# Performance work log

Measured on AMD Instinct MI355X. Metric: run time of the kernel, lower is better.

Reference implementation:

```python
import jax, jax.numpy as jnp
import numpy as np

B, C, H, W = 8, 256, 64, 64
NH, FF, L, K = 8, 1024, 3, 64
THR = 0.5
DH = C // NH
SCALE = 1.0 / float(np.sqrt(DH))
N = H * W


def setup_inputs() -> dict:
    key = jax.random.key(0)
    ks = jax.random.split(key, 16)
    s = 0.02
    rn = lambda k, shape: (jax.random.normal(k, shape, jnp.float32) * s)
    return {
        "x": jax.random.normal(ks[0], (B, C, H, W), jnp.float32),
        "y": jax.random.normal(ks[1], (B, C, H, W), jnp.float32),
        "proj_w": rn(ks[2], (C, 2 * C)), "proj_b": rn(ks[3], (C,)),
        "sal_w": rn(ks[4], (1, C)), "sal_b": rn(ks[5], (1,)),
        "soft_w": rn(ks[6], (2, K, C)), "soft_b": rn(ks[7], (2, K)),
        "attn_in_w": rn(ks[8], (2, L, 3 * C, C)), "attn_in_b": rn(ks[9], (2, L, 3 * C)),
        "attn_out_w": rn(ks[10], (2, L, C, C)), "attn_out_b": rn(ks[11], (2, L, C)),
        "n1_g": jnp.ones((2, L, C), jnp.float32), "n1_b": jnp.zeros((2, L, C), jnp.float32),
        "ffn_w1": rn(ks[12], (2, L, FF, C)), "ffn_b1": rn(ks[13], (2, L, FF)),
        "ffn_w2": rn(ks[14], (2, L, C, FF)), "ffn_b2": rn(ks[15], (2, L, C)),
        "n2_g": jnp.ones((2, L, C), jnp.float32), "n2_b": jnp.zeros((2, L, C), jnp.float32),
    }


def _ln(t, g, b, eps=1e-5):
    m = t.mean(-1, keepdims=True)
    v = ((t - m) ** 2).mean(-1, keepdims=True)
    return (t - m) / jnp.sqrt(v + eps) * g + b


def _layers(q, kv, p, side):
    # q: [B,N,C] pixel queries, kv: [B,K,C] soft-pooled tokens
    for l in range(L):
        iw, ib = p["attn_in_w"][side, l], p["attn_in_b"][side, l]
        qq = (q @ iw[:C].T + ib[:C]).reshape(B, -1, NH, DH)
        kk = (kv @ iw[C:2 * C].T + ib[C:2 * C]).reshape(B, K, NH, DH)
        vv = (kv @ iw[2 * C:].T + ib[2 * C:]).reshape(B, K, NH, DH)
        att = jax.nn.softmax(jnp.einsum('bnhd,bkhd->bhnk', qq, kk) * SCALE, axis=-1)
        o = jnp.einsum('bhnk,bkhd->bnhd', att, vv).reshape(B, -1, C)
        o = o @ p["attn_out_w"][side, l].T + p["attn_out_b"][side, l]
        q = _ln(q + o, p["n1_g"][side, l], p["n1_b"][side, l])
        h = jax.nn.relu(q @ p["ffn_w1"][side, l].T + p["ffn_b1"][side, l])
        h = h @ p["ffn_w2"][side, l].T + p["ffn_b2"][side, l]
        q = _ln(q + h, p["n2_g"][side, l], p["n2_b"][side, l])
    return q


def _forward(x, y, proj_w, proj_b, sal_w, sal_b, soft_w, soft_b,
             attn_in_w, attn_in_b, attn_out_w, attn_out_b, n1_g, n1_b,
             ffn_w1, ffn_b1, ffn_w2, ffn_b2, n2_g, n2_b):
    p = dict(attn_in_w=attn_in_w, attn_in_b=attn_in_b, attn_out_w=attn_out_w,
             attn_out_b=attn_out_b, n1_g=n1_g, n1_b=n1_b, ffn_w1=ffn_w1,
             ffn_b1=ffn_b1, ffn_w2=ffn_w2, ffn_b2=ffn_b2, n2_g=n2_g, n2_b=n2_b)
    xc = jnp.concatenate([x, y], axis=1)                                  # [B,2C,H,W]
    feat = jnp.einsum('oc,bchw->bohw', proj_w, xc) + proj_b[None, :, None, None]
    sal = jnp.einsum('oc,bchw->bohw', sal_w, feat) + sal_b[None, :, None, None]  # [B,1,H,W]
    heat = jax.nn.sigmoid(sal)
    fg_mask = (heat >= THR).reshape(B, 1, N)
    bg_mask = (heat < 1.0 - THR).reshape(B, 1, N)
    fmap = feat.reshape(B, C, N)
    q0 = fmap.transpose(0, 2, 1)                                          # [B,N,C]
    out = fmap
    for side, hm in ((0, heat), (1, 1.0 - heat)):
        wf = feat * hm                                                    # [B,C,H,W]
        sw = (jnp.einsum('kc,bchw->bkhw', soft_w[side], wf)
              + soft_b[side][None, :, None, None]).reshape(B, K, N)       # [B,K,N]
        pool = jnp.einsum('bkn,bcn->bkc', sw, wf.reshape(B, C, N))        # [B,K,C]
        qs = _layers(q0, pool, p, side)                                   # [B,N,C]
        mask = fg_mask if side == 0 else bg_mask
        out = jnp.where(mask, qs.transpose(0, 2, 1), out)
    # per-image skip: if no fg or no bg pixels, keep original feature
    valid = fg_mask.any(axis=(1, 2)) & bg_mask.any(axis=(1, 2))           # [B]
    out = jnp.where(valid[:, None, None], out, fmap)
    return out.reshape(B, C, H, W)


def reference(x, y, proj_w, proj_b, sal_w, sal_b, soft_w, soft_b,
              attn_in_w, attn_in_b, attn_out_w, attn_out_b, n1_g, n1_b,
              ffn_w1, ffn_b1, ffn_w2, ffn_b2, n2_g, n2_b):
    return _forward(x, y, proj_w, proj_b, sal_w, sal_b, soft_w, soft_b,
                    attn_in_w, attn_in_b, attn_out_w, attn_out_b, n1_g, n1_b,
                    ffn_w1, ffn_b1, ffn_w2, ffn_b2, n2_g, n2_b)
```

## Files before the change

### kernel.cpp

```cpp
#include <hip/hip_runtime.h>
#include <stdint.h>

#define B_ 8
#define C_ 256
#define N_ 4096
#define K_ 64
#define NH_ 8
#define FF_ 1024
#define L_ 3
#define M_ (B_*N_)
#define SCALE_ 0.17677669529663687f

typedef float f32x4 __attribute__((ext_vector_type(4)));
typedef __bf16 v8bf __attribute__((ext_vector_type(8)));

__device__ __forceinline__ float b2f(unsigned short h){
  union { uint32_t u; float f; } v; v.u = ((uint32_t)h) << 16; return v.f;
}
__device__ __forceinline__ unsigned short f2b(float f){
  union { float f; uint32_t u; } v; v.f = f;
  uint32_t r = v.u + 0x7fffu + ((v.u >> 16) & 1u);
  return (unsigned short)(r >> 16);
}
__device__ __forceinline__ void gload_lds16(const void* g, void* l){
  __builtin_amdgcn_global_load_lds(
      (const __attribute__((address_space(1))) unsigned int*)g,
      (__attribute__((address_space(3))) unsigned int*)l, 16, 0, 0);
}

__global__ __launch_bounds__(256) void k_f32_to_bf16(const float* __restrict__ src,
                                                     unsigned short* __restrict__ dst, int n){
  int i4 = (blockIdx.x*256 + threadIdx.x)*4;
  if (i4 >= n) return;
  float4 v = *(const float4*)(src + i4);
  uint32_t p0 = (uint32_t)f2b(v.x) | ((uint32_t)f2b(v.y) << 16);
  uint32_t p1 = (uint32_t)f2b(v.z) | ((uint32_t)f2b(v.w) << 16);
  *(uint2*)(dst + i4) = make_uint2(p0, p1);
}

__global__ __launch_bounds__(256) void k_build_xcT(const float* __restrict__ x,
                                                   const float* __restrict__ y,
                                                   unsigned short* __restrict__ xcT){
  __shared__ float t[32][33];
  int b = blockIdx.z;
  int n0 = blockIdx.x*32, c0 = blockIdx.y*32;
  int tx = threadIdx.x, ty = threadIdx.y;
  const float* src = (c0 < 256) ? (x + ((size_t)b*256 + c0)*N_)
                                : (y + ((size_t)b*256 + (c0-256))*N_);
  #pragma unroll
  for (int i = 0; i < 4; i++){
    int cl = ty*4 + i;
    t[cl][tx] = src[(size_t)cl*N_ + n0 + tx];
  }
  __syncthreads();
  #pragma unroll
  for (int i = 0; i < 4; i++){
    int nl = ty*4 + i;
    xcT[((size_t)b*N_ + n0 + nl)*512 + c0 + tx] = f2b(t[tx][nl]);
  }
}

__global__ __launch_bounds__(256) void k_featmir(const float* __restrict__ featT,
                                                 unsigned short* __restrict__ featbf,
                                                 unsigned short* __restrict__ featC){
  __shared__ float t[32][33];
  int b = blockIdx.z;
  int n0 = blockIdx.x*32, c0 = blockIdx.y*32;
  int tx = threadIdx.x, ty = threadIdx.y;
  #pragma unroll
  for (int i = 0; i < 4; i++){
    int nl = ty*4 + i;
    size_t m = (size_t)b*N_ + n0 + nl;
    float v = featT[m*256 + c0 + tx];
    t[nl][tx] = v;
    featbf[m*256 + c0 + tx] = f2b(v);
  }
  __syncthreads();
  #pragma unroll
  for (int i = 0; i < 4; i++){
    int cl = ty*4 + i;
    featC[((size_t)b*256 + c0 + cl)*(size_t)N_ + n0 + tx] = f2b(t[tx][cl]);
  }
}

__global__ __launch_bounds__(512) void k_compute_u(const float* __restrict__ sal_w,
                                                   const float* __restrict__ proj_w,
                                                   const float* __restrict__ proj_b,
                                                   const float* __restrict__ sal_b,
                                                   double* __restrict__ u){
  int c2 = threadIdx.x;
  double acc = 0.0;
  for (int c = 0; c < 256; ++c)
    acc += (double)sal_w[c] * (double)proj_w[(size_t)c*512 + c2];
  u[c2] = acc;
  if (c2 == 0){
    double s0 = (double)sal_b[0];
    for (int c = 0; c < 256; ++c) s0 += (double)sal_w[c] * (double)proj_b[c];
    u[512] = s0;
  }
}

__global__ __launch_bounds__(256) void k_sal_heat(const float* __restrict__ x,
                                                  const float* __restrict__ y,
                                                  const double* __restrict__ u,
                                                  float* __restrict__ heat,
                                                  int* __restrict__ counts){
  int pix = blockIdx.x*256 + threadIdx.x;
  int b = pix >> 12, n = pix & 4095;
  const float* xb = x + (size_t)b*256*N_ + n;
  const float* yb = y + (size_t)b*256*N_ + n;
  double acc = u[512];
  for (int c = 0; c < 256; ++c) acc += u[c]     * (double)xb[(size_t)c*N_];
  for (int c = 0; c < 256; ++c) acc += u[256+c] * (double)yb[(size_t)c*N_];
  float hf = (float)(1.0 / (1.0 + exp(-acc)));
  heat[pix] = hf;
  unsigned long long mfg = __ballot(hf >= 0.5f);
  unsigned long long mbg = __ballot(hf < 0.5f);
  if ((threadIdx.x & 63) == 0){
    atomicAdd(&counts[b*2+0], (int)__popcll(mfg));
    atomicAdd(&counts[b*2+1], (int)__popcll(mbg));
  }
}

template<int EPI>
__global__ __launch_bounds__(256) void k_gemm_bt(
    const unsigned short* __restrict__ A, const unsigned short* __restrict__ W,
    const float* __restrict__ bias, void* __restrict__ out,
    int M, int N, int K){
  __shared__ unsigned short smem[2][2][128*64];
  int tid = threadIdx.x;
  int w = tid >> 6, l = tid & 63;
  int m0 = blockIdx.x * 128, n0 = blockIdx.y * 128;
  int wr = w >> 1, wc = w & 1;
  int lr = l & 15, lk = l >> 4;
  f32x4 acc[4][4] = {};
  int nt = K >> 6;
  #pragma unroll
  for (int i = 0; i < 4; i++){
    int idx = i*256 + tid;
    int row = idx >> 3, su = ((idx & 7) ^ (row & 7))*8;
    gload_lds16(A + (size_t)(m0+row)*K + su, &smem[0][0][idx*8]);
    gload_lds16(W + (size_t)(n0+row)*K + su, &smem[0][1][idx*8]);
  }
  __syncthreads();
  for (int t = 0; t < nt; ++t){
    int cur = t & 1;
    if (t + 1 < nt){
      int k0 = (t + 1) << 6;
      #pragma unroll
      for (int i = 0; i < 4; i++){
        int idx = i*256 + tid;
        int row = idx >> 3, su = ((idx & 7) ^ (row & 7))*8;
        gload_lds16(A + (size_t)(m0+row)*K + k0 + su, &smem[cur^1][0][idx*8]);
        gload_lds16(W + (size_t)(n0+row)*K + k0 + su, &smem[cur^1][1][idx*8]);
      }
    }
    const unsigned short* ldsA = smem[cur][0];
    const unsigned short* ldsB = smem[cur][1];
    #pragma unroll
    for (int kk = 0; kk < 2; kk++){
      v8bf af[4], bfr[4];
      #pragma unroll
      for (int f = 0; f < 4; f++){
        int ra = wr*64 + f*16 + lr;
        int rb2 = wc*64 + f*16 + lr;
        int u = kk*4 + lk;
        af[f]  = *(const v8bf*)(&ldsA[ra*64 + ((u ^ (ra&7))<<3)]);
        bfr[f] = *(const v8bf*)(&ldsB[rb2*64 + ((u ^ (rb2&7))<<3)]);
      }
      #pragma unroll
      for (int fi = 0; fi < 4; fi++)
        #pragma unroll
        for (int fj = 0; fj < 4; fj++)
          acc[fi][fj] = __builtin_amdgcn_mfma_f32_16x16x32_bf16(af[fi], bfr[fj], acc[fi][fj], 0, 0, 0);
    }
    __syncthreads();
  }
  if (EPI == 1 || EPI == 2){
    unsigned short* st = &smem[0][0][0];
    #pragma unroll
    for (int fj = 0; fj < 4; fj++){
      int col = wc*64 + fj*16 + lr;
      float bv = bias[n0 + col];
      #pragma unroll
      for (int fi = 0; fi < 4; fi++){
        int rl = wr*64 + fi*16 + lk*4;
        #pragma unroll
        for (int r = 0; r < 4; r++){
          float v = acc[fi][fj][r] + bv;
          if (EPI == 1) v = fmaxf(v, 0.f);
          st[(rl + r)*136 + col] = f2b(v);
        }
      }
    }
    __syncthreads();
    #pragma unroll
    for (int it = 0; it < 8; it++){
      int idx = it*256 + tid;
      int row = idx >> 4, c8 = (idx & 15)*8;
      *(uint4*)((unsigned short*)out + (size_t)(m0+row)*N + n0 + c8)
          = *(const uint4*)&st[row*136 + c8];
    }
  } else {
    #pragma unroll
    for (int fj = 0; fj < 4; fj++){
      int col = n0 + wc*64 + fj*16 + lr;
      float bv = bias[col];
      #pragma unroll
      for (int fi = 0; fi < 4; fi++){
        int rb = m0 + wr*64 + fi*16 + lk*4;
        #pragma unroll
        for (int r = 0; r < 4; r++){
          float v = acc[fi][fj][r] + bv;
          if (EPI == 3){
            int row = rb + r;
            ((unsigned short*)out)[((size_t)(row>>6)*256 + col)*64 + (row&63)] = f2b(v);
          } else {
            ((float*)out)[(size_t)(rb + r)*N + col] = v;
          }
        }
      }
    }
  }
}

__global__ __launch_bounds__(256) void k_swh(const float* __restrict__ g_all,
                                             const float* __restrict__ heat,
                                             const float* __restrict__ soft_b,
                                             unsigned short* __restrict__ swh){
  __shared__ float gl[64*129];
  __shared__ float hml[64];
  int tid = threadIdx.x;
  int blk = blockIdx.x;
  size_t m0 = (size_t)blk*64;
  int b = (int)(m0 >> 12), n0 = (int)(m0 & 4095);
  #pragma unroll
  for (int i = 0; i < 32; i++){
    int idx = i*256 + tid;
    int row = idx >> 7, col = idx & 127;
    gl[row*129 + col] = g_all[(m0 + row)*128 + col];
  }
  if (tid < 64) hml[tid] = heat[(size_t)b*4096 + n0 + tid];
  __syncthreads();
  int k = tid >> 2, j0 = (tid & 3)*16;
  #pragma unroll
  for (int s = 0; s < 2; s++){
    float sb = soft_b[s*64 + k];
    unsigned short vals[16];
    #pragma unroll
    for (int j = 0; j < 16; j++){
      int n = j0 + j;
      float h = hml[n];
      float hm = s ? (1.0f - h) : h;
      vals[j] = f2b((gl[n*129 + s*64 + k]*hm + sb)*hm);
    }
    unsigned short* dst = swh + (((size_t)b*2 + s)*64 + k)*4096 + n0 + j0;
    uint4 o0, o1;
    o0.x = vals[0] | ((uint32_t)vals[1]<<16);  o0.y = vals[2] | ((uint32_t)vals[3]<<16);
    o0.z = vals[4] | ((uint32_t)vals[5]<<16);  o0.w = vals[6] | ((uint32_t)vals[7]<<16);
    o1.x = vals[8] | ((uint32_t)vals[9]<<16);  o1.y = vals[10]| ((uint32_t)vals[11]<<16);
    o1.z = vals[12]| ((uint32_t)vals[13]<<16); o1.w = vals[14]| ((uint32_t)vals[15]<<16);
    *(uint4*)dst = o0;
    *(uint4*)(dst + 8) = o1;
  }
}

__global__ __launch_bounds__(256) void k_poolgemm(
    const unsigned short* __restrict__ swh, const unsigned short* __restrict__ featC,
    float* __restrict__ pp){
  __shared__ unsigned short ldsA[128*64];
  __shared__ unsigned short ldsB[128*64];
  int tid = threadIdx.x;
  int w = tid >> 6, l = tid & 63;
  int kc = blockIdx.x, nt = blockIdx.y, b = blockIdx.z;
  int wr = w >> 1, wc = w & 1;
  int lr = l & 15, lk = l >> 4;
  const unsigned short* A = swh  + (size_t)b*128*4096 + kc*512;
  const unsigned short* W = featC + ((size_t)b*256 + nt*128)*4096 + kc*512;
  f32x4 acc[4][4] = {};
  for (int k0 = 0; k0 < 512; k0 += 64){
    #pragma unroll
    for (int i = 0; i < 4; i++){
      int idx = i*256 + tid;
      int row = idx >> 3, su = (idx & 7) ^ (row & 7);
      gload_lds16(A + (size_t)row*4096 + k0 + su*8, &ldsA[idx*8]);
    }
    #pragma unroll
    for (int i = 0; i < 4; i++){
      int idx = i*256 + tid;
      int row = idx >> 3, su = (idx & 7) ^ (row & 7);
      gload_lds16(W + (size_t)row*4096 + k0 + su*8, &ldsB[idx*8]);
    }
    __syncthreads();
    #pragma unroll
    for (int kk = 0; kk < 2; kk++){
      v8bf af[4], bfr[4];
      #pragma unroll
      for (int f = 0; f < 4; f++){
        int ra = wr*64 + f*16 + lr;
        int rb2 = wc*64 + f*16 + lr;
        int u = kk*4 + lk;
        af[f]  = *(const v8bf*)(&ldsA[ra*64 + ((u ^ (ra&7))<<3)]);
        bfr[f] = *(const v8bf*)(&ldsB[rb2*64 + ((u ^ (rb2&7))<<3)]);
      }
      #pragma unroll
      for (int fi = 0; fi < 4; fi++)
        #pragma unroll
        for (int fj = 0; fj < 4; fj++)
          acc[fi][fj] = __builtin_amdgcn_mfma_f32_16x16x32_bf16(af[fi], bfr[fj], acc[fi][fj], 0, 0, 0);
    }
    __syncthreads();
  }
  float* dst = pp + ((size_t)kc*8 + b)*128*256;
  #pragma unroll
  for (int fj = 0; fj < 4; fj++){
    int col = nt*128 + wc*64 + fj*16 + lr;
    #pragma unroll
    for (int fi = 0; fi < 4; fi++){
      int rb = wr*64 + fi*16 + lk*4;
      #pragma unroll
      for (int r = 0; r < 4; r++)
        dst[(size_t)(rb + r)*256 + col] = acc[fi][fj][r];
    }
  }
}

__global__ __launch_bounds__(256) void k_pool2b(const float* __restrict__ pp,
                                                unsigned short* __restrict__ pool_bf_s){
  int bk = blockIdx.x, side = blockIdx.y, c = threadIdx.x;
  int b = bk >> 6, k = bk & 63;
  float s = 0.f;
  #pragma unroll
  for (int kc = 0; kc < 8; kc++)
    s += pp[(((size_t)kc*8 + b)*128 + side*64 + k)*256 + c];
  pool_bf_s[((size_t)side*512 + bk)*256 + c] = f2b(s);
}

__global__ __launch_bounds__(256) void k_attn2(
    const unsigned short* __restrict__ qq, const unsigned short* __restrict__ kk,
    const unsigned short* __restrict__ vvT, unsigned short* __restrict__ obf){
  __shared__ unsigned short sk[64*256];
  __shared__ unsigned short svT[256*64];
  __shared__ unsigned short sp[4][16*64];
  __shared__ unsigned short sow[4][16*32];
  int tid = threadIdx.x, w = tid >> 6, l = tid & 63;
  int blk = blockIdx.x, b = blk >> 6;
  int l15 = l & 15, lg = l >> 4;
  const uint4* ksrc = (const uint4*)(kk + (size_t)b*64*256);
  #pragma unroll
  for (int i = 0; i < 8; i++){
    int u = i*256 + tid;
    int row = u >> 5, j = u & 31;
    *(uint4*)&sk[row*256 + ((j ^ (row&7))<<3)] = ksrc[u];
  }
  const uint4* vsrc = (const uint4*)(vvT + (size_t)b*256*64);
  #pragma unroll
  for (int i = 0; i < 8; i++){
    int u = i*256 + tid;
    int row = u >> 3, j = u & 7;
    *(uint4*)&svT[row*64 + ((j ^ (row&7))<<3)] = vsrc[u];
  }
  __syncthreads();
  size_t qrow = (size_t)blk*64 + w*16 + l15;
  for (int h = 0; h < 8; h++){
    v8bf aq = *(const v8bf*)(qq + qrow*256 + h*32 + lg*8);
    f32x4 s[4];
    #pragma unroll
    for (int kt = 0; kt < 4; kt++){
      int row = kt*16 + l15;
      v8bf bk = *(const v8bf*)&sk[row*256 + (((h*4 + lg) ^ (row&7))<<3)];
      f32x4 z = {};
      s[kt] = __builtin_amdgcn_mfma_f32_16x16x32_bf16(aq, bk, z, 0, 0, 0);
    }
    #pragma unroll
    for (int r = 0; r < 4; r++){
      float v0 = s[0][r]*SCALE_, v1 = s[1][r]*SCALE_;
      float v2 = s[2][r]*SCALE_, v3 = s[3][r]*SCALE_;
      float mx = fmaxf(fmaxf(v0, v1), fmaxf(v2, v3));
      mx = fmaxf(mx, __shfl_xor(mx, 1));
      mx = fmaxf(mx, __shfl_xor(mx, 2));
      mx = fmaxf(mx, __shfl_xor(mx, 4));
      mx = fmaxf(mx, __shfl_xor(mx, 8));
      float e0 = __expf(v0-mx), e1 = __expf(v1-mx);
      float e2 = __expf(v2-mx), e3 = __expf(v3-mx);
      float sum = e0+e1+e2+e3;
      sum += __shfl_xor(sum, 1); sum += __shfl_xor(sum, 2);
      sum += __shfl_xor(sum, 4); sum += __shfl_xor(sum, 8);
      float inv = 1.0f/sum;
      s[0][r] = e0*inv; s[1][r] = e1*inv; s[2][r] = e2*inv; s[3][r] = e3*inv;
    }
    #pragma unroll
    for (int kt = 0; kt < 4; kt++){
      int colu = kt*2 + (l15>>3);
      #pragma unroll
      for (int r = 0; r < 4; r++){
        int row = lg*4 + r;
        sp[w][row*64 + ((colu ^ (row&7))<<3) + (l&7)] = f2b(s[kt][r]);
      }
    }
    f32x4 o[2] = {};
    #pragma unroll
    for (int k2 = 0; k2 < 2; k2++){
      v8bf pa = *(const v8bf*)&sp[w][l15*64 + (((k2*4 + lg) ^ (l15&7))<<3)];
      #pragma unroll
      for (int dt = 0; dt < 2; dt++){
        int vrow = h*32 + dt*16 + l15;
        v8bf bv = *(const v8bf*)&svT[vrow*64 + (((k2*4 + lg) ^ (vrow&7))<<3)];
        o[dt] = __builtin_amdgcn_mfma_f32_16x16x32_bf16(pa, bv, o[dt], 0, 0, 0);
      }
    }
    #pragma unroll
    for (int dt = 0; dt < 2; dt++)
      #pragma unroll
      for (int r = 0; r < 4; r++)
        sow[w][(lg*4 + r)*32 + dt*16 + l15] = f2b(o[dt][r]);
    uint4 ov = *(const uint4*)&sow[w][l15*32 + lg*8];
    *(uint4*)(obf + qrow*256 + h*32 + lg*8) = ov;
  }
}

template<int RF32>
__global__ __launch_bounds__(256) void k_ln2(
    const void* __restrict__ resid, const unsigned short* __restrict__ delta,
    const float* __restrict__ g, const float* __restrict__ bta,
    unsigned short* __restrict__ qout){
  int wv = threadIdx.x >> 6, l = threadIdx.x & 63;
  size_t m = (size_t)blockIdx.x*4 + wv;
  uint2 dv = *(const uint2*)(delta + m*256 + l*4);
  float d0 = b2f((unsigned short)(dv.x & 0xffff)), d1 = b2f((unsigned short)(dv.x >> 16));
  float d2 = b2f((unsigned short)(dv.y & 0xffff)), d3 = b2f((unsigned short)(dv.y >> 16));
  float x0, x1, x2, x3;
  if (RF32){
    float4 rv = *(const float4*)((const float*)resid + m*256 + l*4);
    x0 = rv.x+d0; x1 = rv.y+d1; x2 = rv.z+d2; x3 = rv.w+d3;
  } else {
    uint2 rv = *(const uint2*)((const unsigned short*)resid + m*256 + l*4);
    x0 = b2f((unsigned short)(rv.x & 0xffff)) + d0;
    x1 = b2f((unsigned short)(rv.x >> 16)) + d1;
    x2 = b2f((unsigned short)(rv.y & 0xffff)) + d2;
    x3 = b2f((unsigned short)(rv.y >> 16)) + d3;
  }
  float s = x0+x1+x2+x3;
  float ss = x0*x0+x1*x1+x2*x2+x3*x3;
  #pragma unroll
  for (int off = 32; off; off >>= 1){
    s  += __shfl_xor(s, off);
    ss += __shfl_xor(ss, off);
  }
  float mean = s * (1.0f/256.0f);
  float var = ss * (1.0f/256.0f) - mean*mean;
  float rstd = 1.0f / sqrtf(var + 1e-5f);
  float4 gv = *(const float4*)(g + l*4);
  float4 bv = *(const float4*)(bta + l*4);
  float y0 = (x0-mean)*rstd*gv.x + bv.x;
  float y1 = (x1-mean)*rstd*gv.y + bv.y;
  float y2 = (x2-mean)*rstd*gv.z + bv.z;
  float y3 = (x3-mean)*rstd*gv.w + bv.w;
  uint32_t p0 = (uint32_t)f2b(y0) | ((uint32_t)f2b(y1)<<16);
  uint32_t p1 = (uint32_t)f2b(y2) | ((uint32_t)f2b(y3)<<16);
  *(uint2*)(qout + m*256 + l*4) = make_uint2(p0,p1);
}

__global__ __launch_bounds__(256) void k_select(
    const unsigned short* __restrict__ qA, const unsigned short* __restrict__ qB,
    const float* __restrict__ featT, const float* __restrict__ heat,
    const int* __restrict__ counts, float* __restrict__ out){
  __shared__ float t[32][33];
  int b = blockIdx.z;
  int n0 = blockIdx.x*32, c0 = blockIdx.y*32;
  int tx = threadIdx.x, ty = threadIdx.y;
  bool valid = (counts[b*2] > 0) && (counts[b*2+1] > 0);
  #pragma unroll
  for (int i = 0; i < 4; i++){
    int nl = ty*4+i;
    size_t m = (size_t)b*4096 + n0 + nl;
    float v;
    if (!valid) v = featT[m*256 + c0 + tx];
    else {
      bool fg = heat[(size_t)b*4096 + n0 + nl] >= 0.5f;
      v = fg ? b2f(qA[m*256 + c0 + tx]) : b2f(qB[m*256 + c0 + tx]);
    }
    t[nl][tx] = v;
  }
  __syncthreads();
  #pragma unroll
  for (int i = 0; i < 4; i++){
    int cl = ty*4+i;
    out[((size_t)b*256 + c0 + cl)*4096 + n0 + tx] = t[tx][cl];
  }
}

extern "C" void kernel_launch(void* const* d_in, const int* in_sizes, int n_in,
                              void* d_out, int out_size, void* d_ws, size_t ws_size,
                              hipStream_t stream){
  const float* x         = (const float*)d_in[0];
  const float* y         = (const float*)d_in[1];
  const float* proj_w    = (const float*)d_in[2];
  const float* proj_b    = (const float*)d_in[3];
  const float* sal_w     = (const float*)d_in[4];
  const float* sal_b     = (const float*)d_in[5];
  const float* soft_w    = (const float*)d_in[6];
  const float* soft_b    = (const float*)d_in[7];
  const float* attn_in_w = (const float*)d_in[8];
  const float* attn_in_b = (const float*)d_in[9];
  const float* attn_out_w= (const float*)d_in[10];
  const float* attn_out_b= (const float*)d_in[11];
  const float* n1_g      = (const float*)d_in[12];
  const float* n1_b      = (const float*)d_in[13];
  const float* ffn_w1    = (const float*)d_in[14];
  const float* ffn_b1    = (const float*)d_in[15];
  const float* ffn_w2    = (const float*)d_in[16];
  const float* ffn_b2    = (const float*)d_in[17];
  const float* n2_g      = (const float*)d_in[18];
  const float* n2_b      = (const float*)d_in[19];
  float* out = (float*)d_out;

  char* p = (char*)d_ws;
  auto alloc = [&](size_t bytes){ char* r = p; p += (bytes + 255) & ~(size_t)255; return r; };
  unsigned short* hbf   = (unsigned short*)alloc((size_t)M_*FF_*2);
  unsigned short* xcT   = hbf;
  unsigned short* qq_bf = hbf;
  float* featT = (float*)alloc((size_t)M_*C_*4);
  unsigned short* qAb = (unsigned short*)alloc((size_t)M_*C_*2);
  unsigned short* swh = qAb;
  unsigned short* qBb = (unsigned short*)alloc((size_t)M_*C_*2);
  unsigned short* obf = (unsigned short*)alloc((size_t)M_*C_*2);
  unsigned short* featC = obf;
  unsigned short* featbf = (unsigned short*)alloc((size_t)M_*C_*2);
  unsigned short* tmpb = (unsigned short*)alloc((size_t)M_*C_*2);
  float* g_all = (float*)tmpb;
  float* pp    = (float*)alloc((size_t)8*8*128*256*4);
  unsigned short* pool_bf_s = (unsigned short*)alloc((size_t)2*512*256*2);
  unsigned short* kk_bf = (unsigned short*)alloc((size_t)B_*K_*C_*2);
  unsigned short* vvT_bf= (unsigned short*)alloc((size_t)B_*C_*K_*2);
  float* heat = (float*)alloc((size_t)B_*N_*4);
  double* u   = (double*)alloc(513*8);
  int* counts = (int*)alloc(64);
  float* zbias = (float*)alloc(512);
  unsigned short* projw_bf = (unsigned short*)alloc((size_t)C_*512*2);
  unsigned short* aiw_bf = (unsigned short*)alloc((size_t)2*L_*768*C_*2);
  unsigned short* aow_bf = (unsigned short*)alloc((size_t)2*L_*C_*C_*2);
  unsigned short* f1w_bf = (unsigned short*)alloc((size_t)2*L_*FF_*C_*2);
  unsigned short* f2w_bf = (unsigned short*)alloc((size_t)2*L_*C_*FF_*2);
  unsigned short* sw2_bf = (unsigned short*)alloc((size_t)2*K_*C_*2);

  hipMemsetAsync(counts, 0, 64, stream);
  hipMemsetAsync(zbias, 0, 512, stream);
  k_compute_u<<<1, 512, 0, stream>>>(sal_w, proj_w, proj_b, sal_b, u);
  k_sal_heat<<<128, 256, 0, stream>>>(x, y, u, heat, counts);

  auto conv = [&](const float* s, unsigned short* d, size_t n){
    k_f32_to_bf16<<<(unsigned)((n/4 + 255)/256), 256, 0, stream>>>(s, d, (int)n);
  };
  conv(proj_w,     projw_bf, (size_t)C_*512);
  conv(attn_in_w,  aiw_bf,   (size_t)2*L_*768*C_);
  conv(attn_out_w, aow_bf,   (size_t)2*L_*C_*C_);
  conv(ffn_w1,     f1w_bf,   (size_t)2*L_*FF_*C_);
  conv(ffn_w2,     f2w_bf,   (size_t)2*L_*C_*FF_);
  conv(soft_w,     sw2_bf,   (size_t)2*K_*C_);

  k_build_xcT<<<dim3(N_/32, 512/32, B_), dim3(32,8), 0, stream>>>(x, y, xcT);
  k_gemm_bt<0><<<dim3(M_/128, C_/128), 256, 0, stream>>>(xcT, projw_bf, proj_b, featT, M_, C_, 512);
  k_featmir<<<dim3(N_/32, C_/32, B_), dim3(32,8), 0, stream>>>(featT, featbf, featC);

  k_gemm_bt<0><<<dim3(M_/128, 1), 256, 0, stream>>>(featbf, sw2_bf, zbias, g_all, M_, 128, C_);
  k_swh<<<M_/64, 256, 0, stream>>>(g_all, heat, soft_b, swh);
  k_poolgemm<<<dim3(8, 2, B_), 256, 0, stream>>>(swh, featC, pp);
  k_pool2b<<<dim3(512, 2), 256, 0, stream>>>(pp, pool_bf_s);

  for (int side = 0; side < 2; ++side){
    unsigned short* qb = side ? qBb : qAb;
    const unsigned short* poolS = pool_bf_s + (size_t)side*512*256;
    for (int lyr = 0; lyr < L_; ++lyr){
      int sl = side*L_ + lyr;
      const unsigned short* iw = aiw_bf + (size_t)sl*768*C_;
      const float* ib = attn_in_b + (size_t)sl*768;
      const unsigned short* qin = (lyr == 0) ? featbf : qb;
      k_gemm_bt<2><<<dim3(M_/128, C_/128), 256, 0, stream>>>(qin, iw, ib, qq_bf, M_, C_, C_);
      k_gemm_bt<2><<<dim3((B_*K_)/128, C_/128), 256, 0, stream>>>(poolS, iw + 256*C_, ib + 256, kk_bf, B_*K_, C_, C_);
      k_gemm_bt<3><<<dim3((B_*K_)/128, C_/128), 256, 0, stream>>>(poolS, iw + 512*C_, ib + 512, vvT_bf, B_*K_, C_, C_);
      k_attn2<<<M_/64, 256, 0, stream>>>(qq_bf, kk_bf, vvT_bf, obf);
      k_gemm_bt<2><<<dim3(M_/128, C_/128), 256, 0, stream>>>(obf, aow_bf + (size_t)sl*C_*C_, attn_out_b + (size_t)sl*C_, tmpb, M_, C_, C_);
      if (lyr == 0)
        k_ln2<1><<<M_/4, 256, 0, stream>>>(featT, tmpb, n1_g + (size_t)sl*C_, n1_b + (size_t)sl*C_, qb);
      else
        k_ln2<0><<<M_/4, 256, 0, stream>>>(qb, tmpb, n1_g + (size_t)sl*C_, n1_b + (size_t)sl*C_, qb);
      k_gemm_bt<1><<<dim3(M_/128, FF_/128), 256, 0, stream>>>(qb, f1w_bf + (size_t)sl*FF_*C_, ffn_b1 + (size_t)sl*FF_, hbf, M_, FF_, C_);
      k_gemm_bt<2><<<dim3(M_/128, C_/128), 256, 0, stream>>>(hbf, f2w_bf + (size_t)sl*C_*FF_, ffn_b2 + (size_t)sl*C_, tmpb, M_, C_, FF_);
      k_ln2<0><<<M_/4, 256, 0, stream>>>(qb, tmpb, n2_g + (size_t)sl*C_, n2_b + (size_t)sl*C_, qb);
    }
  }
  k_select<<<dim3(N_/32, C_/32, B_), dim3(32,8), 0, stream>>>(qAb, qBb, featT, heat, counts, out);
}
```

Measured before the change: 923.6 us.

## Fuse FFN up/down GEMMs into one kernel and split saliency reduction

Replaces the two FFN GEMM launches with one fused kernel. Each block keeps a 128-row activation tile in LDS, computes 64-wide chunks of the ReLU hidden layer, and immediately accumulates them into the output, so the M×1024 hidden tensor never goes to global memory. Separately, the saliency dot product is split across 16 channel chunks into double partials plus a reduction kernel, to raise parallelism beyond 128 blocks. The fused kernel uses about 144KB of LDS, which allows only one block per CU with no load/compute overlap, and it has only 256 blocks.

Result: slower. 970.6 us (+5.1%).

```diff
diff --git a/kernel.cpp b/kernel.cpp
--- a/kernel.cpp
+++ b/kernel.cpp
@@ -100,18 +100,32 @@
   }
 }
 
-__global__ __launch_bounds__(256) void k_sal_heat(const float* __restrict__ x,
+__global__ __launch_bounds__(256) void k_sal_part(const float* __restrict__ x,
                                                   const float* __restrict__ y,
                                                   const double* __restrict__ u,
-                                                  float* __restrict__ heat,
-                                                  int* __restrict__ counts){
+                                                  double* __restrict__ part){
   int pix = blockIdx.x*256 + threadIdx.x;
+  int cc = blockIdx.y;
   int b = pix >> 12, n = pix & 4095;
-  const float* xb = x + (size_t)b*256*N_ + n;
-  const float* yb = y + (size_t)b*256*N_ + n;
+  int c0 = cc*32;
+  const float* src = (c0 < 256) ? (x + ((size_t)b*256 + c0)*N_ + n)
+                                : (y + ((size_t)b*256 + (c0-256))*N_ + n);
+  const double* uu = u + c0;
+  double acc = 0.0;
+  #pragma unroll 8
+  for (int c = 0; c < 32; ++c) acc += uu[c] * (double)src[(size_t)c*N_];
+  part[(size_t)cc*32768 + pix] = acc;
+}
+
+__global__ __launch_bounds__(256) void k_sal_red(const double* __restrict__ part,
+                                                 const double* __restrict__ u,
+                                                 float* __restrict__ heat,
+                                                 int* __restrict__ counts){
+  int pix = blockIdx.x*256 + threadIdx.x;
+  int b = pix >> 12;
   double acc = u[512];
-  for (int c = 0; c < 256; ++c) acc += u[c]     * (double)xb[(size_t)c*N_];
-  for (int c = 0; c < 256; ++c) acc += u[256+c] * (double)yb[(size_t)c*N_];
+  #pragma unroll
+  for (int cc = 0; cc < 16; cc++) acc += part[(size_t)cc*32768 + pix];
   float hf = (float)(1.0 / (1.0 + exp(-acc)));
   heat[pix] = hf;
   unsigned long long mfg = __ballot(hf >= 0.5f);
@@ -221,6 +235,125 @@
         }
       }
     }
+  }
+}
+
+__global__ __launch_bounds__(256) void k_ffn(
+    const unsigned short* __restrict__ qb, const unsigned short* __restrict__ W1g,
+    const float* __restrict__ b1g, const unsigned short* __restrict__ W2g,
+    const float* __restrict__ b2g, unsigned short* __restrict__ outb){
+  __shared__ unsigned short smem[73728];
+  unsigned short* sA  = smem;
+  unsigned short* sW1 = smem + 32768;
+  unsigned short* sW2 = smem + 49152;
+  unsigned short* sH  = smem + 65536;
+  int tid = threadIdx.x, w = tid >> 6, l = tid & 63;
+  int m0 = blockIdx.x * 128;
+  int wrM = w >> 1, wcF = w & 1;
+  int lr = l & 15, lk = l >> 4;
+  #pragma unroll
+  for (int i = 0; i < 16; i++){
+    int idx = i*256 + tid;
+    int row = idx >> 5, g = idx & 31;
+    int su = (g & 24) | ((g & 7) ^ (row & 7));
+    gload_lds16(qb + (size_t)(m0+row)*256 + su*8, &sA[idx*8]);
+  }
+  f32x4 acc[4][8] = {};
+  for (int cc = 0; cc < 16; ++cc){
+    int f0 = cc*64;
+    #pragma unroll
+    for (int i = 0; i < 8; i++){
+      int idx = i*256 + tid;
+      int row = idx >> 5, g = idx & 31;
+      int su = (g & 24) | ((g & 7) ^ (row & 7));
+      gload_lds16(W1g + (size_t)(f0+row)*256 + su*8, &sW1[idx*8]);
+    }
+    #pragma unroll
+    for (int i = 0; i < 8; i++){
+      int idx = i*256 + tid;
+      int row = idx >> 3, g = idx & 7;
+      int su = g ^ (row & 7);
+      gload_lds16(W2g + (size_t)row*1024 + f0 + su*8, &sW2[idx*8]);
+    }
+    __syncthreads();
+    f32x4 hacc[4][2] = {};
+    #pragma unroll
+    for (int ks = 0; ks < 8; ks++){
+      v8bf af[4], bf[2];
+      int g = ks*4 + lk;
+      #pragma unroll
+      for (int f = 0; f < 4; f++){
+        int ra = wrM*64 + f*16 + lr;
+        af[f] = *(const v8bf*)&sA[ra*256 + (((g & 24) | ((g & 7) ^ (ra & 7)))<<3)];
+      }
+      #pragma unroll
+      for (int f = 0; f < 2; f++){
+        int rf = wcF*32 + f*16 + lr;
+        bf[f] = *(const v8bf*)&sW1[rf*256 + (((g & 24) | ((g & 7) ^ (rf & 7)))<<3)];
+      }
+      #pragma unroll
+      for (int fi = 0; fi < 4; fi++)
+        #pragma unroll
+        for (int fj = 0; fj < 2; fj++)
+          hacc[fi][fj] = __builtin_amdgcn_mfma_f32_16x16x32_bf16(af[fi], bf[fj], hacc[fi][fj], 0, 0, 0);
+    }
+    #pragma unroll
+    for (int fj = 0; fj < 2; fj++){
+      int fc = wcF*32 + fj*16 + lr;
+      float b1v = b1g[f0 + fc];
+      #pragma unroll
+      for (int fi = 0; fi < 4; fi++){
+        int mr0 = wrM*64 + fi*16 + lk*4;
+        #pragma unroll
+        for (int r = 0; r < 4; r++){
+          float v = fmaxf(hacc[fi][fj][r] + b1v, 0.f);
+          int mr = mr0 + r;
+          sH[mr*64 + (((fc >> 3) ^ (mr & 7))<<3) + (fc & 7)] = f2b(v);
+        }
+      }
+    }
+    __syncthreads();
+    #pragma unroll
+    for (int ks2 = 0; ks2 < 2; ks2++){
+      v8bf ha[4], wb[8];
+      int g = ks2*4 + lk;
+      #pragma unroll
+      for (int f = 0; f < 4; f++){
+        int rh = wrM*64 + f*16 + lr;
+        ha[f] = *(const v8bf*)&sH[rh*64 + ((g ^ (rh & 7))<<3)];
+      }
+      #pragma unroll
+      for (int f = 0; f < 8; f++){
+        int rc = wcF*128 + f*16 + lr;
+        wb[f] = *(const v8bf*)&sW2[rc*64 + ((g ^ (rc & 7))<<3)];
+      }
+      #pragma unroll
+      for (int fi = 0; fi < 4; fi++)
+        #pragma unroll
+        for (int fc = 0; fc < 8; fc++)
+          acc[fi][fc] = __builtin_amdgcn_mfma_f32_16x16x32_bf16(ha[fi], wb[fc], acc[fi][fc], 0, 0, 0);
+    }
+    __syncthreads();
+  }
+  unsigned short* st = smem;
+  #pragma unroll
+  for (int fc = 0; fc < 8; fc++){
+    int col = wcF*128 + fc*16 + lr;
+    float bv = b2g[col];
+    #pragma unroll
+    for (int fi = 0; fi < 4; fi++){
+      int rl = wrM*64 + fi*16 + lk*4;
+      #pragma unroll
+      for (int r = 0; r < 4; r++)
+        st[(rl + r)*264 + col] = f2b(acc[fi][fc][r] + bv);
+    }
+  }
+  __syncthreads();
+  #pragma unroll
+  for (int it = 0; it < 16; it++){
+    int idx = it*256 + tid;
+    int row = idx >> 5, c8 = (idx & 31)*8;
+    *(uint4*)(outb + (size_t)(m0+row)*256 + c8) = *(const uint4*)&st[row*264 + c8];
   }
 }
 
@@ -530,6 +663,7 @@
   unsigned short* tmpb = (unsigned short*)alloc((size_t)M_*C_*2);
   float* g_all = (float*)tmpb;
   float* pp    = (float*)alloc((size_t)8*8*128*256*4);
+  double* salp = (double*)pp;
   unsigned short* pool_bf_s = (unsigned short*)alloc((size_t)2*512*256*2);
   unsigned short* kk_bf = (unsigned short*)alloc((size_t)B_*K_*C_*2);
   unsigned short* vvT_bf= (unsigned short*)alloc((size_t)B_*C_*K_*2);
@@ -547,7 +681,8 @@
   hipMemsetAsync(counts, 0, 64, stream);
   hipMemsetAsync(zbias, 0, 512, stream);
   k_compute_u<<<1, 512, 0, stream>>>(sal_w, proj_w, proj_b, sal_b, u);
-  k_sal_heat<<<128, 256, 0, stream>>>(x, y, u, heat, counts);
+  k_sal_part<<<dim3(128, 16), 256, 0, stream>>>(x, y, u, salp);
+  k_sal_red<<<128, 256, 0, stream>>>(salp, u, heat, counts);
 
   auto conv = [&](const float* s, unsigned short* d, size_t n){
     k_f32_to_bf16<<<(unsigned)((n/4 + 255)/256), 256, 0, stream>>>(s, d, (int)n);
@@ -585,8 +720,8 @@
         k_ln2<1><<<M_/4, 256, 0, stream>>>(featT, tmpb, n1_g + (size_t)sl*C_, n1_b + (size_t)sl*C_, qb);
       else
         k_ln2<0><<<M_/4, 256, 0, stream>>>(qb, tmpb, n1_g + (size_t)sl*C_, n1_b + (size_t)sl*C_, qb);
-      k_gemm_bt<1><<<dim3(M_/128, FF_/128), 256, 0, stream>>>(qb, f1w_bf + (size_t)sl*FF_*C_, ffn_b1 + (size_t)sl*FF_, hbf, M_, FF_, C_);
-      k_gemm_bt<2><<<dim3(M_/128, C_/128), 256, 0, stream>>>(hbf, f2w_bf + (size_t)sl*C_*FF_, ffn_b2 + (size_t)sl*C_, tmpb, M_, C_, FF_);
+      k_ffn<<<M_/128, 256, 0, stream>>>(qb, f1w_bf + (size_t)sl*FF_*C_, ffn_b1 + (size_t)sl*FF_,
+                                        f2w_bf + (size_t)sl*C_*FF_, ffn_b2 + (size_t)sl*C_, tmpb);
       k_ln2<0><<<M_/4, 256, 0, stream>>>(qb, tmpb, n2_g + (size_t)sl*C_, n2_b + (size_t)sl*C_, qb);
     }
   }
```
